# Kernel tuning notes

Hardware: AMD Instinct MI355X
Metric: run time of the kernel (lower is better)

The kernel has to match this reference:

```python
import jax, jax.numpy as jnp
import numpy as np

N, L, H, E = 4, 4096, 8, 64
CHUNK = 128  # chunk size for the blocked causal scan
EPS = 1e-6


def elu_feature_map(x):
    # phi(x) = elu(x) + 1 (default feature map of fast-transformers)
    return jax.nn.elu(x) + 1.0


def causal_dot_product(Q, K, V, chunk=CHUNK):
    """out[n,l,h,:] = sum_{s<=l} (Q[n,l,h,:].K[n,s,h,:]) * V[n,s,h,:].
    Chunked scan over the [E,M] KV state: O(N L H E M) without an [L,L] matrix."""
    n, l, h, e = Q.shape
    m = V.shape[-1]
    nc = l // chunk

    def to_chunks(x):
        # [n, l, h, d] -> [nc, n, h, chunk, d]
        return x.reshape(n, nc, chunk, h, x.shape[-1]).transpose(1, 0, 3, 2, 4)

    q, k, v = to_chunks(Q), to_chunks(K), to_chunks(V)
    tril = jnp.tril(jnp.ones((chunk, chunk), dtype=Q.dtype))

    def step(S, xs):  # S: [n, h, e, m] running sum of k v^T
        qc, kc, vc = xs  # [n, h, chunk, e/m]
        inter = jnp.einsum('nhce,nhem->nhcm', qc, S)
        attn = jnp.einsum('nhce,nhde->nhcd', qc, kc) * tril  # intra-chunk causal
        intra = jnp.einsum('nhcd,nhdm->nhcm', attn, vc)
        S = S + jnp.einsum('nhce,nhcm->nhem', kc, vc)
        return S, inter + intra

    S0 = jnp.zeros((n, h, e, m), dtype=Q.dtype)
    _, out = jax.lax.scan(step, S0, (q, k, v))  # [nc, n, h, chunk, m]
    return out.transpose(1, 0, 3, 2, 4).reshape(n, l, h, m)


def setup_inputs() -> dict:
    key = jax.random.key(0)
    k1, k2, k3 = jax.random.split(key, 3)
    return {
        'queries': jax.random.normal(k1, (N, L, H, E), jnp.float32),
        'keys': jax.random.normal(k2, (N, L, H, E), jnp.float32),
        'values': jax.random.normal(k3, (N, L, H, E), jnp.float32),
        'key_lengths': jnp.ones((N, L), jnp.float32),  # float length mask
    }


def reference(queries, keys, values, key_lengths):
    Q = elu_feature_map(queries)
    K = elu_feature_map(keys) * key_lengths[:, :, None, None]
    # denominator: Z[n,l,h] = 1 / (Q[n,l,h] . cumsum_s<=l K[n,s,h] + eps)
    Z = 1.0 / (jnp.einsum('nlhe,nlhe->nlh', Q, jnp.cumsum(K, axis=1)) + EPS)
    V_new = causal_dot_product(Q, K, values)
    return V_new * Z[:, :, :, None]
```

## Files before the change

kernel.cpp:

```cpp
#include <hip/hip_runtime.h>
#include <math.h>

#define NN 4
#define LL 4096
#define HH 8
#define EE 64
#define CHK 64
#define GSUP 2
#define SUPC (CHK*GSUP)
#define NSUP (LL/SUPC)
#define NH (NN*HH)
#define NBLK (NH*NSUP)
#define NCH64 (LL/CHK)
#define EPSF 1e-6f

typedef float f32x4 __attribute__((ext_vector_type(4)));
typedef __bf16 bf16x8 __attribute__((ext_vector_type(8)));

__device__ __forceinline__ float phi_map(float x) {
  return x > 0.0f ? x + 1.0f : __expf(x);
}

#define MFMA(a, b, c) __builtin_amdgcn_mfma_f32_16x16x32_bf16((a), (b), (c), 0, 0, 0)

__device__ __forceinline__ int swz64(int row, int d) {
  return row * 64 + (d & 7) + 8 * ((d >> 3) ^ ((row >> 2) & 7));
}
__device__ __forceinline__ int frag64(int row, int blk) {
  return row * 64 + 8 * (blk ^ ((row >> 2) & 7));
}

#define K1_ISSUE(J, BUF) { \
  const int l0i = (sc * GSUP + (J)) * CHK; \
  _Pragma("unroll") for (int it = 0; it < 4; ++it) { \
    int f = t + 256 * it; int d = f >> 4; int c4 = (f & 15) << 2; \
    size_t gb = (((size_t)n * LL + (size_t)(l0i + d)) * HH + h) * EE + c4; \
    pk[BUF][it] = *(const float4*)(Kg + gb); \
    pv[BUF][it] = *(const float4*)(Vg + gb); \
    pl[BUF][it] = KLg[n * LL + l0i + d]; } }

#define K1_STAGE(BUF) { \
  _Pragma("unroll") for (int it = 0; it < 4; ++it) { \
    int f = t + 256 * it; int d = f >> 4; int c4 = (f & 15) << 2; \
    float klr = pl[BUF][it]; float4 kk = pk[BUF][it]; float4 vv = pv[BUF][it]; \
    float ka[4] = {phi_map(kk.x) * klr, phi_map(kk.y) * klr, phi_map(kk.z) * klr, phi_map(kk.w) * klr}; \
    float va[4] = {vv.x, vv.y, vv.z, vv.w}; \
    _Pragma("unroll") for (int jj = 0; jj < 4; ++jj) { \
      sKt[BUF][swz64(c4 + jj, d)] = (__bf16)ka[jj]; \
      sVt[BUF][swz64(c4 + jj, d)] = (__bf16)va[jj]; } } }

__global__ __launch_bounds__(256, 2) void k_chunksums(
    const float* __restrict__ Kg, const float* __restrict__ Vg,
    const float* __restrict__ KLg, __bf16* __restrict__ ScG, __bf16* __restrict__ KscG)
{
  __shared__ __bf16 sKt[2][4096];
  __shared__ __bf16 sVt[2][4096];
  const int g = blockIdx.x;
  const int sc = g % NSUP;
  const int nh = g / NSUP;
  const int h = nh % HH;
  const int n = nh / HH;
  const int t = threadIdx.x;
  const int w = t >> 6;
  const int lane = t & 63;
  const int lg = lane >> 4;
  const int li = lane & 15;

  float4 pk[2][4], pv[2][4];
  float pl[2][4];

  K1_ISSUE(0, 0);
  K1_STAGE(0);

  f32x4 acc[4];
  #pragma unroll
  for (int nt = 0; nt < 4; ++nt) acc[nt] = (f32x4){0.f, 0.f, 0.f, 0.f};

  bf16x8 ones;
  #pragma unroll
  for (int i = 0; i < 8; ++i) ones[i] = (__bf16)1.0f;

  #pragma unroll
  for (int j = 0; j < GSUP; ++j) {
    if (j + 1 < GSUP) K1_ISSUE(j + 1, (j + 1) & 1);
    __syncthreads();

    bf16x8 aV0 = *(const bf16x8*)&sVt[j & 1][frag64(16 * w + li, lg)];
    bf16x8 aV1 = *(const bf16x8*)&sVt[j & 1][frag64(16 * w + li, 4 + lg)];

    f32x4 accK[4];
    #pragma unroll
    for (int nt = 0; nt < 4; ++nt) accK[nt] = (f32x4){0.f, 0.f, 0.f, 0.f};

    #pragma unroll
    for (int nt = 0; nt < 4; ++nt) {
      bf16x8 b0 = *(const bf16x8*)&sKt[j & 1][frag64(li + 16 * nt, lg)];
      bf16x8 b1 = *(const bf16x8*)&sKt[j & 1][frag64(li + 16 * nt, 4 + lg)];
      acc[nt] = MFMA(aV0, b0, acc[nt]);
      acc[nt] = MFMA(aV1, b1, acc[nt]);
      if (w == 0) {
        accK[nt] = MFMA(ones, b0, accK[nt]);
        accK[nt] = MFMA(ones, b1, accK[nt]);
      }
    }
    if (w == 0 && lg == 0) {
      #pragma unroll
      for (int nt = 0; nt < 4; ++nt)
        KscG[(size_t)(g * GSUP + j) * 64 + li + 16 * nt] = (__bf16)accK[nt][0];
    }
    if (j + 1 < GSUP) K1_STAGE((j + 1) & 1);
  }

  __bf16* sp = ScG + (size_t)g * 4096;
  #pragma unroll
  for (int nt = 0; nt < 4; ++nt)
    #pragma unroll
    for (int reg = 0; reg < 4; ++reg)
      sp[(16 * w + 4 * lg + reg) * 64 + li + 16 * nt] = (__bf16)acc[nt][reg];
}

__global__ __launch_bounds__(256) void k_prefix(
    __bf16* __restrict__ Sc, __bf16* __restrict__ Ksc)
{
  const int bid = blockIdx.x;
  const int t = threadIdx.x;
  if (bid < NH * 16) {
    const int nh = bid >> 4;
    const int strip = bid & 15;
    const int entry = strip * 256 + t;
    __bf16 v[NSUP];
    #pragma unroll
    for (int c = 0; c < NSUP; ++c)
      v[c] = Sc[((size_t)(nh * NSUP + c) << 12) + entry];
    float run = 0.0f;
    #pragma unroll
    for (int c = 0; c < NSUP; ++c) {
      Sc[((size_t)(nh * NSUP + c) << 12) + entry] = (__bf16)run;
      run += (float)v[c];
    }
  } else {
    const int idx = (bid - NH * 16) * 256 + t;
    const int nh = idx >> 6;
    const int e = idx & 63;
    __bf16 v[NCH64];
    #pragma unroll
    for (int c = 0; c < NCH64; ++c)
      v[c] = Ksc[((size_t)(nh * NCH64 + c) << 6) + e];
    float run = 0.0f;
    #pragma unroll
    for (int c = 0; c < NCH64; ++c) {
      Ksc[((size_t)(nh * NCH64 + c) << 6) + e] = (__bf16)run;
      run += (float)v[c];
    }
  }
}

#define P2_ISSUE(CC) { \
  const int l0i = (sc * GSUP + (CC)) * CHK; \
  _Pragma("unroll") for (int it = 0; it < 4; ++it) { \
    int f = t + 256 * it; int d = f >> 4; int c4 = (f & 15) << 2; \
    size_t gb = (((size_t)n * LL + (size_t)(l0i + d)) * HH + h) * EE + c4; \
    pk[it] = *(const float4*)(Kg + gb); \
    pv[it] = *(const float4*)(Vg + gb); \
    pl[it] = KLg[n * LL + l0i + d]; } \
  { const float* qr = Qg + (((size_t)n * LL + (size_t)(l0i + arow)) * HH + h) * EE; \
    pq[0] = *(const float4*)(qr + 8 * lg); \
    pq[1] = *(const float4*)(qr + 8 * lg + 4); \
    pq[2] = *(const float4*)(qr + 32 + 8 * lg); \
    pq[3] = *(const float4*)(qr + 32 + 8 * lg + 4); } }

#define P2_STAGE(QB) { \
  _Pragma("unroll") for (int it = 0; it < 4; ++it) { \
    int f = t + 256 * it; int d = f >> 4; int c4 = (f & 15) << 2; \
    float klr = pl[it]; float4 kk = pk[it]; float4 vv = pv[it]; \
    float ka[4] = {phi_map(kk.x) * klr, phi_map(kk.y) * klr, phi_map(kk.z) * klr, phi_map(kk.w) * klr}; \
    float va[4] = {vv.x, vv.y, vv.z, vv.w}; \
    _Pragma("unroll") for (int jj = 0; jj < 4; ++jj) { \
      sKe[swz64(d, c4 + jj)] = (__bf16)ka[jj]; \
      sKt[swz64(c4 + jj, d)] = (__bf16)ka[jj]; \
      sVt[swz64(c4 + jj, d)] = (__bf16)va[jj]; } } \
  { float4 q0 = pq[0], q1 = pq[1], q2 = pq[2], q3 = pq[3]; \
    bf16x8 a0, a1; \
    a0[0] = (__bf16)phi_map(q0.x); a0[1] = (__bf16)phi_map(q0.y); \
    a0[2] = (__bf16)phi_map(q0.z); a0[3] = (__bf16)phi_map(q0.w); \
    a0[4] = (__bf16)phi_map(q1.x); a0[5] = (__bf16)phi_map(q1.y); \
    a0[6] = (__bf16)phi_map(q1.z); a0[7] = (__bf16)phi_map(q1.w); \
    a1[0] = (__bf16)phi_map(q2.x); a1[1] = (__bf16)phi_map(q2.y); \
    a1[2] = (__bf16)phi_map(q2.z); a1[3] = (__bf16)phi_map(q2.w); \
    a1[4] = (__bf16)phi_map(q3.x); a1[5] = (__bf16)phi_map(q3.y); \
    a1[6] = (__bf16)phi_map(q3.z); a1[7] = (__bf16)phi_map(q3.w); \
    aQ[QB][0] = a0; aQ[QB][1] = a1; } }

__global__ __launch_bounds__(256, 2) void k_pass2(
    const float* __restrict__ Qg, const float* __restrict__ Kg,
    const float* __restrict__ Vg, const float* __restrict__ KLg,
    const __bf16* __restrict__ Sp, const __bf16* __restrict__ Ksp,
    float* __restrict__ Og)
{
  __shared__ __bf16 sKe[4096];
  __shared__ __bf16 sKt[4096];
  __shared__ __bf16 sVt[4096];
  __shared__ __bf16 sU[4096];

  const int g = blockIdx.x;
  const int sc = g % NSUP;
  const int nh = g / NSUP;
  const int h = nh % HH;
  const int n = nh / HH;
  const int t = threadIdx.x;
  const int w = t >> 6;
  const int lane = t & 63;
  const int lg = lane >> 4;
  const int li = lane & 15;
  const int arow = 16 * w + li;

  float4 pk[4], pv[4], pq[4];
  float pl[4];
  bf16x8 aQ[2][2];

  {
    const bf16x8* sp8 = (const bf16x8*)(Sp + (size_t)g * 4096);
    bf16x8 s0 = sp8[2 * t];
    bf16x8 s1 = sp8[2 * t + 1];
    int m = t >> 2, eb = (t & 3) * 2;
    *(bf16x8*)&sU[frag64(m, eb)] = s0;
    *(bf16x8*)&sU[frag64(m, eb + 1)] = s1;
  }

  P2_ISSUE(0);
  P2_STAGE(0);

  f32x4 accS[4];

  #pragma unroll
  for (int cc = 0; cc < GSUP; ++cc) {
    __syncthreads();

    if (cc == 0) {
      #pragma unroll
      for (int nt = 0; nt < 4; ++nt)
        #pragma unroll
        for (int reg = 0; reg < 4; ++reg)
          accS[nt][reg] = (float)sU[swz64(16 * w + 4 * lg + reg, li + 16 * nt)];
    }

    if (cc + 1 < GSUP) P2_ISSUE(cc + 1);

    bf16x8 aQ0 = aQ[cc & 1][0], aQ1 = aQ[cc & 1][1];

    f32x4 acc[4];
    #pragma unroll
    for (int nt = 0; nt < 4; ++nt) {
      acc[nt] = (f32x4){0.f, 0.f, 0.f, 0.f};
      bf16x8 b0 = *(const bf16x8*)&sU[frag64(li + 16 * nt, lg)];
      bf16x8 b1 = *(const bf16x8*)&sU[frag64(li + 16 * nt, 4 + lg)];
      acc[nt] = MFMA(aQ0, b0, acc[nt]);
      acc[nt] = MFMA(aQ1, b1, acc[nt]);
    }

    const __bf16* kb = Ksp + (size_t)(g * GSUP + cc) * 64;
    bf16x8 ks0 = *(const bf16x8*)(kb + 8 * lg);
    bf16x8 ks1 = *(const bf16x8*)(kb + 32 + 8 * lg);
    float dv = 0.0f;
    #pragma unroll
    for (int i = 0; i < 8; ++i) {
      dv += (float)aQ0[i] * (float)ks0[i];
      dv += (float)aQ1[i] * (float)ks1[i];
    }
    dv += __shfl_xor(dv, 16);
    dv += __shfl_xor(dv, 32);
    float den[4];
    #pragma unroll
    for (int reg = 0; reg < 4; ++reg) den[reg] = __shfl(dv, 4 * lg + reg);

    __syncthreads();

    float rs[4] = {0.f, 0.f, 0.f, 0.f};
    #pragma unroll
    for (int nt = 0; nt < 4; ++nt) {
      f32x4 at2 = (f32x4){0.f, 0.f, 0.f, 0.f};
      if (nt <= w) {
        bf16x8 b0 = *(const bf16x8*)&sKe[frag64(li + 16 * nt, lg)];
        bf16x8 b1 = *(const bf16x8*)&sKe[frag64(li + 16 * nt, 4 + lg)];
        at2 = MFMA(aQ0, b0, at2);
        at2 = MFMA(aQ1, b1, at2);
      }
      #pragma unroll
      for (int reg = 0; reg < 4; ++reg) {
        int row = 16 * w + 4 * lg + reg;
        int col = li + 16 * nt;
        float av = (col <= row) ? at2[reg] : 0.0f;
        rs[reg] += av;
        sU[swz64(row, col)] = (__bf16)av;
      }
    }

    #pragma unroll
    for (int reg = 0; reg < 4; ++reg) {
      float v = rs[reg];
      v += __shfl_xor(v, 1);
      v += __shfl_xor(v, 2);
      v += __shfl_xor(v, 4);
      v += __shfl_xor(v, 8);
      rs[reg] = v;
    }

    {
      bf16x8 aP0 = *(const bf16x8*)&sU[frag64(arow, lg)];
      bf16x8 aP1 = aP0;
      if (w >= 2) aP1 = *(const bf16x8*)&sU[frag64(arow, 4 + lg)];
      #pragma unroll
      for (int nt = 0; nt < 4; ++nt) {
        bf16x8 bv0 = *(const bf16x8*)&sVt[frag64(li + 16 * nt, lg)];
        acc[nt] = MFMA(aP0, bv0, acc[nt]);
        if (w >= 2) {
          bf16x8 bv1 = *(const bf16x8*)&sVt[frag64(li + 16 * nt, 4 + lg)];
          acc[nt] = MFMA(aP1, bv1, acc[nt]);
        }
      }
    }

    const int l0 = (sc * GSUP + cc) * CHK;
    #pragma unroll
    for (int reg = 0; reg < 4; ++reg) {
      float inv = 1.0f / (den[reg] + rs[reg] + EPSF);
      int row = l0 + 16 * w + 4 * lg + reg;
      size_t ob = (((size_t)n * LL + row) * HH + h) * EE + li;
      #pragma unroll
      for (int nt = 0; nt < 4; ++nt)
        Og[ob + 16 * nt] = acc[nt][reg] * inv;
    }

    if (cc + 1 < GSUP) {
      bf16x8 aV0 = *(const bf16x8*)&sVt[frag64(arow, lg)];
      bf16x8 aV1 = *(const bf16x8*)&sVt[frag64(arow, 4 + lg)];
      #pragma unroll
      for (int nt = 0; nt < 4; ++nt) {
        bf16x8 bk0 = *(const bf16x8*)&sKt[frag64(li + 16 * nt, lg)];
        bf16x8 bk1 = *(const bf16x8*)&sKt[frag64(li + 16 * nt, 4 + lg)];
        accS[nt] = MFMA(aV0, bk0, accS[nt]);
        accS[nt] = MFMA(aV1, bk1, accS[nt]);
        #pragma unroll
        for (int reg = 0; reg < 4; ++reg)
          sU[swz64(16 * w + 4 * lg + reg, li + 16 * nt)] = (__bf16)accS[nt][reg];
      }

      __syncthreads();
      P2_STAGE((cc + 1) & 1);
    }
  }
}

extern "C" void kernel_launch(void* const* d_in, const int* in_sizes, int n_in,
                              void* d_out, int out_size, void* d_ws, size_t ws_size,
                              hipStream_t stream) {
  const float* Qg  = (const float*)d_in[0];
  const float* Kg  = (const float*)d_in[1];
  const float* Vg  = (const float*)d_in[2];
  const float* KLg = (const float*)d_in[3];
  float* Og = (float*)d_out;

  __bf16* Sc  = (__bf16*)d_ws;
  __bf16* Ksc = (__bf16*)((char*)d_ws + (size_t)NBLK * 4096 * 2);

  hipLaunchKernelGGL(k_chunksums, dim3(NBLK), dim3(256), 0, stream, Kg, Vg, KLg, Sc, Ksc);
  hipLaunchKernelGGL(k_prefix, dim3(NH * 16 + 8), dim3(256), 0, stream, Sc, Ksc);
  hipLaunchKernelGGL(k_pass2, dim3(NBLK), dim3(256), 0, stream, Qg, Kg, Vg, KLg, Sc, Ksc, Og);
}
```

Measured before the change: 51.99 us.

## Double-buffer pass2 LDS, transpose MFMA operands, and enlarge superchunks to four

Raises the number of 64-row chunks per block from 2 to 4, which halves the block count. It double-buffers the K/V/state LDS tiles so one barrier per chunk suffices. The MFMA operand order is swapped so each lane holds whole output rows, which enables float4 global stores, bf16x4 LDS stores, and per-wave private P tiles without cross-row shuffles. The running state accumulator is now seeded directly from global memory. This costs roughly double the LDS per block, which may lower occupancy, and gives fewer blocks for parallelism.

```diff
diff --git a/kernel.cpp b/kernel.cpp
--- a/kernel.cpp
+++ b/kernel.cpp
@@ -6,9 +6,8 @@
 #define HH 8
 #define EE 64
 #define CHK 64
-#define GSUP 2
-#define SUPC (CHK*GSUP)
-#define NSUP (LL/SUPC)
+#define GSUP 4
+#define NSUP 16
 #define NH (NN*HH)
 #define NBLK (NH*NSUP)
 #define NCH64 (LL/CHK)
@@ -16,6 +15,7 @@
 
 typedef float f32x4 __attribute__((ext_vector_type(4)));
 typedef __bf16 bf16x8 __attribute__((ext_vector_type(8)));
+typedef __bf16 bf16x4 __attribute__((ext_vector_type(4)));
 
 __device__ __forceinline__ float phi_map(float x) {
   return x > 0.0f ? x + 1.0f : __expf(x);
@@ -56,8 +56,8 @@
   __shared__ __bf16 sKt[2][4096];
   __shared__ __bf16 sVt[2][4096];
   const int g = blockIdx.x;
-  const int sc = g % NSUP;
-  const int nh = g / NSUP;
+  const int sc = g & (NSUP - 1);
+  const int nh = g >> 4;
   const int h = nh % HH;
   const int n = nh / HH;
   const int t = threadIdx.x;
@@ -65,6 +65,7 @@
   const int lane = t & 63;
   const int lg = lane >> 4;
   const int li = lane & 15;
+  const int arow = 16 * w + li;
 
   float4 pk[2][4], pv[2][4];
   float pl[2][4];
@@ -85,8 +86,8 @@
     if (j + 1 < GSUP) K1_ISSUE(j + 1, (j + 1) & 1);
     __syncthreads();
 
-    bf16x8 aV0 = *(const bf16x8*)&sVt[j & 1][frag64(16 * w + li, lg)];
-    bf16x8 aV1 = *(const bf16x8*)&sVt[j & 1][frag64(16 * w + li, 4 + lg)];
+    bf16x8 bV0 = *(const bf16x8*)&sVt[j & 1][frag64(arow, lg)];
+    bf16x8 bV1 = *(const bf16x8*)&sVt[j & 1][frag64(arow, 4 + lg)];
 
     f32x4 accK[4];
     #pragma unroll
@@ -94,13 +95,13 @@
 
     #pragma unroll
     for (int nt = 0; nt < 4; ++nt) {
-      bf16x8 b0 = *(const bf16x8*)&sKt[j & 1][frag64(li + 16 * nt, lg)];
-      bf16x8 b1 = *(const bf16x8*)&sKt[j & 1][frag64(li + 16 * nt, 4 + lg)];
-      acc[nt] = MFMA(aV0, b0, acc[nt]);
-      acc[nt] = MFMA(aV1, b1, acc[nt]);
+      bf16x8 a0 = *(const bf16x8*)&sKt[j & 1][frag64(li + 16 * nt, lg)];
+      bf16x8 a1 = *(const bf16x8*)&sKt[j & 1][frag64(li + 16 * nt, 4 + lg)];
+      acc[nt] = MFMA(a0, bV0, acc[nt]);
+      acc[nt] = MFMA(a1, bV1, acc[nt]);
       if (w == 0) {
-        accK[nt] = MFMA(ones, b0, accK[nt]);
-        accK[nt] = MFMA(ones, b1, accK[nt]);
+        accK[nt] = MFMA(ones, a0, accK[nt]);
+        accK[nt] = MFMA(ones, a1, accK[nt]);
       }
     }
     if (w == 0 && lg == 0) {
@@ -113,10 +114,12 @@
 
   __bf16* sp = ScG + (size_t)g * 4096;
   #pragma unroll
-  for (int nt = 0; nt < 4; ++nt)
-    #pragma unroll
-    for (int reg = 0; reg < 4; ++reg)
-      sp[(16 * w + 4 * lg + reg) * 64 + li + 16 * nt] = (__bf16)acc[nt][reg];
+  for (int nt = 0; nt < 4; ++nt) {
+    bf16x4 sv;
+    #pragma unroll
+    for (int reg = 0; reg < 4; ++reg) sv[reg] = (__bf16)acc[nt][reg];
+    *(bf16x4*)(sp + arow * 64 + 16 * nt + 4 * lg) = sv;
+  }
 }
 
 __global__ __launch_bounds__(256) void k_prefix(
@@ -175,10 +178,12 @@
     float klr = pl[it]; float4 kk = pk[it]; float4 vv = pv[it]; \
     float ka[4] = {phi_map(kk.x) * klr, phi_map(kk.y) * klr, phi_map(kk.z) * klr, phi_map(kk.w) * klr}; \
     float va[4] = {vv.x, vv.y, vv.z, vv.w}; \
+    bf16x4 kv4; \
+    kv4[0] = (__bf16)ka[0]; kv4[1] = (__bf16)ka[1]; kv4[2] = (__bf16)ka[2]; kv4[3] = (__bf16)ka[3]; \
+    *(bf16x4*)&sKe[QB][d * 64 + 8 * ((c4 >> 3) ^ ((d >> 2) & 7)) + (c4 & 7)] = kv4; \
     _Pragma("unroll") for (int jj = 0; jj < 4; ++jj) { \
-      sKe[swz64(d, c4 + jj)] = (__bf16)ka[jj]; \
-      sKt[swz64(c4 + jj, d)] = (__bf16)ka[jj]; \
-      sVt[swz64(c4 + jj, d)] = (__bf16)va[jj]; } } \
+      sKt[QB][swz64(c4 + jj, d)] = (__bf16)ka[jj]; \
+      sVt[QB][swz64(c4 + jj, d)] = (__bf16)va[jj]; } } \
   { float4 q0 = pq[0], q1 = pq[1], q2 = pq[2], q3 = pq[3]; \
     bf16x8 a0, a1; \
     a0[0] = (__bf16)phi_map(q0.x); a0[1] = (__bf16)phi_map(q0.y); \
@@ -197,14 +202,15 @@
     const __bf16* __restrict__ Sp, const __bf16* __restrict__ Ksp,
     float* __restrict__ Og)
 {
-  __shared__ __bf16 sKe[4096];
-  __shared__ __bf16 sKt[4096];
-  __shared__ __bf16 sVt[4096];
-  __shared__ __bf16 sU[4096];
+  __shared__ __bf16 sKe[2][4096];
+  __shared__ __bf16 sKt[2][4096];
+  __shared__ __bf16 sVt[2][4096];
+  __shared__ __bf16 sU[2][4096];
+  __shared__ __bf16 sP[4][1024];
 
   const int g = blockIdx.x;
-  const int sc = g % NSUP;
-  const int nh = g / NSUP;
+  const int sc = g & (NSUP - 1);
+  const int nh = g >> 4;
   const int h = nh % HH;
   const int n = nh / HH;
   const int t = threadIdx.x;
@@ -223,39 +229,38 @@
     bf16x8 s0 = sp8[2 * t];
     bf16x8 s1 = sp8[2 * t + 1];
     int m = t >> 2, eb = (t & 3) * 2;
-    *(bf16x8*)&sU[frag64(m, eb)] = s0;
-    *(bf16x8*)&sU[frag64(m, eb + 1)] = s1;
+    *(bf16x8*)&sU[0][frag64(m, eb)] = s0;
+    *(bf16x8*)&sU[0][frag64(m, eb + 1)] = s1;
+  }
+
+  f32x4 accS[4];
+  #pragma unroll
+  for (int nt = 0; nt < 4; ++nt) {
+    bf16x4 sv = *(const bf16x4*)(Sp + (size_t)g * 4096 + arow * 64 + 16 * nt + 4 * lg);
+    #pragma unroll
+    for (int reg = 0; reg < 4; ++reg) accS[nt][reg] = (float)sv[reg];
   }
 
   P2_ISSUE(0);
   P2_STAGE(0);
 
-  f32x4 accS[4];
-
   #pragma unroll
   for (int cc = 0; cc < GSUP; ++cc) {
+    const int cb = cc & 1, nb = cb ^ 1;
     __syncthreads();
 
-    if (cc == 0) {
-      #pragma unroll
-      for (int nt = 0; nt < 4; ++nt)
-        #pragma unroll
-        for (int reg = 0; reg < 4; ++reg)
-          accS[nt][reg] = (float)sU[swz64(16 * w + 4 * lg + reg, li + 16 * nt)];
-    }
-
     if (cc + 1 < GSUP) P2_ISSUE(cc + 1);
 
-    bf16x8 aQ0 = aQ[cc & 1][0], aQ1 = aQ[cc & 1][1];
+    bf16x8 aQ0 = aQ[cb][0], aQ1 = aQ[cb][1];
 
     f32x4 acc[4];
     #pragma unroll
     for (int nt = 0; nt < 4; ++nt) {
       acc[nt] = (f32x4){0.f, 0.f, 0.f, 0.f};
-      bf16x8 b0 = *(const bf16x8*)&sU[frag64(li + 16 * nt, lg)];
-      bf16x8 b1 = *(const bf16x8*)&sU[frag64(li + 16 * nt, 4 + lg)];
-      acc[nt] = MFMA(aQ0, b0, acc[nt]);
-      acc[nt] = MFMA(aQ1, b1, acc[nt]);
+      bf16x8 aS0 = *(const bf16x8*)&sU[cb][frag64(li + 16 * nt, lg)];
+      bf16x8 aS1 = *(const bf16x8*)&sU[cb][frag64(li + 16 * nt, 4 + lg)];
+      acc[nt] = MFMA(aS0, aQ0, acc[nt]);
+      acc[nt] = MFMA(aS1, aQ1, acc[nt]);
     }
 
     const __bf16* kb = Ksp + (size_t)(g * GSUP + cc) * 64;
@@ -269,84 +274,72 @@
     }
     dv += __shfl_xor(dv, 16);
     dv += __shfl_xor(dv, 32);
-    float den[4];
-    #pragma unroll
-    for (int reg = 0; reg < 4; ++reg) den[reg] = __shfl(dv, 4 * lg + reg);
-
-    __syncthreads();
-
-    float rs[4] = {0.f, 0.f, 0.f, 0.f};
+
+    f32x4 at2[4];
+    #pragma unroll
+    for (int nt = 0; nt < 4; ++nt) at2[nt] = (f32x4){0.f, 0.f, 0.f, 0.f};
+    for (int nt = 0; nt <= w; ++nt) {
+      bf16x8 aK0 = *(const bf16x8*)&sKe[cb][frag64(li + 16 * nt, lg)];
+      bf16x8 aK1 = *(const bf16x8*)&sKe[cb][frag64(li + 16 * nt, 4 + lg)];
+      at2[nt] = MFMA(aK0, aQ0, at2[nt]);
+      at2[nt] = MFMA(aK1, aQ1, at2[nt]);
+    }
+
+    float rs = 0.0f;
     #pragma unroll
     for (int nt = 0; nt < 4; ++nt) {
-      f32x4 at2 = (f32x4){0.f, 0.f, 0.f, 0.f};
-      if (nt <= w) {
-        bf16x8 b0 = *(const bf16x8*)&sKe[frag64(li + 16 * nt, lg)];
-        bf16x8 b1 = *(const bf16x8*)&sKe[frag64(li + 16 * nt, 4 + lg)];
-        at2 = MFMA(aQ0, b0, at2);
-        at2 = MFMA(aQ1, b1, at2);
-      }
+      bf16x4 pw;
       #pragma unroll
       for (int reg = 0; reg < 4; ++reg) {
-        int row = 16 * w + 4 * lg + reg;
-        int col = li + 16 * nt;
-        float av = (col <= row) ? at2[reg] : 0.0f;
-        rs[reg] += av;
-        sU[swz64(row, col)] = (__bf16)av;
-      }
-    }
-
-    #pragma unroll
-    for (int reg = 0; reg < 4; ++reg) {
-      float v = rs[reg];
-      v += __shfl_xor(v, 1);
-      v += __shfl_xor(v, 2);
-      v += __shfl_xor(v, 4);
-      v += __shfl_xor(v, 8);
-      rs[reg] = v;
-    }
+        int kk = 16 * nt + 4 * lg + reg;
+        float av = (kk <= arow) ? at2[nt][reg] : 0.0f;
+        rs += av;
+        pw[reg] = (__bf16)av;
+      }
+      *(bf16x4*)&sP[w][li * 64 + 8 * ((2 * nt + (lg >> 1)) ^ (li & 7)) + 4 * (lg & 1)] = pw;
+    }
+    rs += __shfl_xor(rs, 16);
+    rs += __shfl_xor(rs, 32);
 
     {
-      bf16x8 aP0 = *(const bf16x8*)&sU[frag64(arow, lg)];
-      bf16x8 aP1 = aP0;
-      if (w >= 2) aP1 = *(const bf16x8*)&sU[frag64(arow, 4 + lg)];
+      bf16x8 bP0 = *(const bf16x8*)&sP[w][li * 64 + 8 * (lg ^ (li & 7))];
+      bf16x8 bP1 = *(const bf16x8*)&sP[w][li * 64 + 8 * ((4 + lg) ^ (li & 7))];
       #pragma unroll
       for (int nt = 0; nt < 4; ++nt) {
-        bf16x8 bv0 = *(const bf16x8*)&sVt[frag64(li + 16 * nt, lg)];
-        acc[nt] = MFMA(aP0, bv0, acc[nt]);
-        if (w >= 2) {
-          bf16x8 bv1 = *(const bf16x8*)&sVt[frag64(li + 16 * nt, 4 + lg)];
-          acc[nt] = MFMA(aP1, bv1, acc[nt]);
-        }
+        bf16x8 aV0 = *(const bf16x8*)&sVt[cb][frag64(li + 16 * nt, lg)];
+        bf16x8 aV1 = *(const bf16x8*)&sVt[cb][frag64(li + 16 * nt, 4 + lg)];
+        acc[nt] = MFMA(aV0, bP0, acc[nt]);
+        acc[nt] = MFMA(aV1, bP1, acc[nt]);
       }
     }
 
     const int l0 = (sc * GSUP + cc) * CHK;
-    #pragma unroll
-    for (int reg = 0; reg < 4; ++reg) {
-      float inv = 1.0f / (den[reg] + rs[reg] + EPSF);
-      int row = l0 + 16 * w + 4 * lg + reg;
-      size_t ob = (((size_t)n * LL + row) * HH + h) * EE + li;
-      #pragma unroll
-      for (int nt = 0; nt < 4; ++nt)
-        Og[ob + 16 * nt] = acc[nt][reg] * inv;
+    {
+      float inv = 1.0f / (dv + rs + EPSF);
+      size_t ob = (((size_t)n * LL + (size_t)(l0 + arow)) * HH + h) * EE;
+      #pragma unroll
+      for (int nt = 0; nt < 4; ++nt) {
+        float4 o = make_float4(acc[nt][0] * inv, acc[nt][1] * inv,
+                               acc[nt][2] * inv, acc[nt][3] * inv);
+        *(float4*)(Og + ob + 16 * nt + 4 * lg) = o;
+      }
     }
 
     if (cc + 1 < GSUP) {
-      bf16x8 aV0 = *(const bf16x8*)&sVt[frag64(arow, lg)];
-      bf16x8 aV1 = *(const bf16x8*)&sVt[frag64(arow, 4 + lg)];
+      bf16x8 bV0 = *(const bf16x8*)&sVt[cb][frag64(arow, lg)];
+      bf16x8 bV1 = *(const bf16x8*)&sVt[cb][frag64(arow, 4 + lg)];
       #pragma unroll
       for (int nt = 0; nt < 4; ++nt) {
-        bf16x8 bk0 = *(const bf16x8*)&sKt[frag64(li + 16 * nt, lg)];
-        bf16x8 bk1 = *(const bf16x8*)&sKt[frag64(li + 16 * nt, 4 + lg)];
-        accS[nt] = MFMA(aV0, bk0, accS[nt]);
-        accS[nt] = MFMA(aV1, bk1, accS[nt]);
+        bf16x8 aKt0 = *(const bf16x8*)&sKt[cb][frag64(li + 16 * nt, lg)];
+        bf16x8 aKt1 = *(const bf16x8*)&sKt[cb][frag64(li + 16 * nt, 4 + lg)];
+        accS[nt] = MFMA(aKt0, bV0, accS[nt]);
+        accS[nt] = MFMA(aKt1, bV1, accS[nt]);
+        bf16x4 sw;
         #pragma unroll
-        for (int reg = 0; reg < 4; ++reg)
-          sU[swz64(16 * w + 4 * lg + reg, li + 16 * nt)] = (__bf16)accS[nt][reg];
-      }
-
-      __syncthreads();
-      P2_STAGE((cc + 1) & 1);
+        for (int reg = 0; reg < 4; ++reg) sw[reg] = (__bf16)accS[nt][reg];
+        *(bf16x4*)&sU[nb][arow * 64 + 8 * ((2 * nt + (lg >> 1)) ^ ((arow >> 2) & 7)) + 4 * (lg & 1)] = sw;
+      }
+      P2_STAGE(nb);
     }
   }
 }
```

After: 47.34 us, median of 2. -9.0%, faster.
